# Kernel optimization log

Hardware: AMD Instinct MI355X
Metric: run time of the kernel (lower is better)

Reference implementation:

```python
import jax, jax.numpy as jnp
import numpy as np

B, T, D, K = 8, 2048, 384, 64

def setup_inputs() -> dict:
    key = jax.random.key(0)
    k1, k2, k3, k4 = jax.random.split(key, 4)
    x = jax.random.normal(k1, (B, T, D), dtype=jnp.float32)
    # torch nn.Linear default init scale ~ 1/sqrt(fan_in); use scaled normals
    Wq = jax.random.normal(k2, (D, K), dtype=jnp.float32) / np.sqrt(D)
    Wk = jax.random.normal(k3, (D, K), dtype=jnp.float32) / np.sqrt(D)
    Wv = jax.random.normal(k4, (D, D), dtype=jnp.float32) / np.sqrt(D)
    return {"x": x, "Wq": Wq, "Wk": Wk, "Wv": Wv}

def reference(x, Wq, Wk, Wv):
    # x: (B,T,D)
    q = jnp.einsum('btd,dk->btk', x, Wq)      # (B,T,K)
    k = jnp.einsum('btd,dk->btk', x, Wk)      # (B,T,K)
    v = jnp.einsum('btd,de->bte', x, Wv)      # (B,T,D)
    scores = jnp.einsum('bqk,bsk->bqs', q, k) / jnp.sqrt(jnp.float32(K))  # (B,T,T)
    causal = jnp.tril(jnp.ones((T, T), dtype=bool))
    scores = jnp.where(causal, scores, -jnp.inf)
    weights = jax.nn.softmax(scores, axis=-1)
    out = jnp.einsum('bqs,bse->bqe', weights, v)  # (B,T,D)
    return out
```

## Files before the change

kernel.cpp:

```cpp
#include <hip/hip_runtime.h>

#define TT 2048
#define DD 384

typedef float f32x4 __attribute__((ext_vector_type(4)));
typedef float f32x16 __attribute__((ext_vector_type(16)));
typedef short s16x8 __attribute__((ext_vector_type(8)));
typedef short s16x2 __attribute__((ext_vector_type(2)));
typedef unsigned int u32x4 __attribute__((ext_vector_type(4)));

typedef __attribute__((address_space(3))) unsigned char* as3p;
typedef const __attribute__((address_space(1))) unsigned char* as1p;
#define GLLDS(gsrc, ldst) __builtin_amdgcn_global_load_lds((as1p)(gsrc), (as3p)(ldst), 16, 0, 0)

static __device__ __forceinline__ unsigned short f2bf(float f) {
    unsigned int u = __builtin_bit_cast(unsigned int, f);
    u = (u + 0x7fffu + ((u >> 16) & 1u)) >> 16;
    return (unsigned short)u;
}
static __device__ __forceinline__ unsigned int pk2(float a, float b) {
#if __has_builtin(__builtin_amdgcn_cvt_pk_bf16_f32)
    s16x2 t = __builtin_amdgcn_cvt_pk_bf16_f32(a, b);
    return __builtin_bit_cast(unsigned int, t);
#else
    unsigned int ua = __builtin_bit_cast(unsigned int, a);
    unsigned int ub = __builtin_bit_cast(unsigned int, b);
    ua = (ua + 0x7fffu + ((ua >> 16) & 1u)) >> 16;
    ub = (ub + 0x7fffu + ((ub >> 16) & 1u)) & 0xffff0000u;
    return ua | ub;
#endif
}

__global__ __launch_bounds__(256, 2) void qkv_gemm(
    const float* __restrict__ x, const float* __restrict__ Wq,
    const float* __restrict__ Wk, const float* __restrict__ Wv,
    unsigned short* __restrict__ qo, unsigned short* __restrict__ ko,
    unsigned short* __restrict__ vto)
{
    __shared__ __align__(16) unsigned short lds[16384];
    const int tid = threadIdx.x;
    const int l   = tid & 63;
    const int w   = tid >> 6;
    const int si  = l & 15;
    const int qq  = l >> 4;
    const int m0  = blockIdx.x * 128;
    const int nb  = blockIdx.y;
    const int wr  = w >> 1, wc = w & 1;

    const int bn = tid & 127;
    const int bk = (tid >> 7) * 16;
    const float* wsrc; int ldw;
    if (nb == 0) { wsrc = (bn < 64) ? (Wq + bn) : (Wk + (bn - 64)); ldw = 64; }
    else         { wsrc = Wv + (nb - 1) * 128 + bn;                 ldw = 384; }

    f32x4 acc[4][4];
    #pragma unroll
    for (int rt = 0; rt < 4; ++rt)
        #pragma unroll
        for (int ct = 0; ct < 4; ++ct) acc[rt][ct] = (f32x4){0.f, 0.f, 0.f, 0.f};

    for (int kt = 0; kt < 12; ++kt) {
        const int k0 = kt * 32;
        #pragma unroll
        for (int i = 0; i < 2; ++i) {
            const int u = tid + 256 * i, r = u >> 2, c = u & 3;
            const float* xp = x + (size_t)(m0 + r) * DD + k0 + c * 8;
            f32x4 x0 = *(const f32x4*)xp;
            f32x4 x1 = *(const f32x4*)(xp + 4);
            s16x8 av;
            av[0] = (short)f2bf(x0[0]); av[1] = (short)f2bf(x0[1]);
            av[2] = (short)f2bf(x0[2]); av[3] = (short)f2bf(x0[3]);
            av[4] = (short)f2bf(x1[0]); av[5] = (short)f2bf(x1[1]);
            av[6] = (short)f2bf(x1[2]); av[7] = (short)f2bf(x1[3]);
            *(s16x8*)&lds[r * 32 + ((c ^ (r & 3)) * 8)] = av;
        }
        {
            float t[16];
            #pragma unroll
            for (int j = 0; j < 16; ++j) t[j] = wsrc[(size_t)(k0 + bk + j) * ldw];
            #pragma unroll
            for (int jj = 0; jj < 2; ++jj) {
                s16x8 bv;
                #pragma unroll
                for (int j = 0; j < 8; ++j) bv[j] = (short)f2bf(t[jj * 8 + j]);
                const int ch = (tid >> 7) * 2 + jj;
                *(s16x8*)&lds[4096 + bn * 32 + ((ch ^ (bn & 3)) * 8)] = bv;
            }
        }
        __syncthreads();

        s16x8 af[4], bf[4];
        #pragma unroll
        for (int rt = 0; rt < 4; ++rt) {
            const int row = wr * 64 + rt * 16 + si;
            af[rt] = *(const s16x8*)&lds[row * 32 + ((qq ^ (row & 3)) * 8)];
        }
        #pragma unroll
        for (int ct = 0; ct < 4; ++ct) {
            const int col = wc * 64 + ct * 16 + si;
            bf[ct] = *(const s16x8*)&lds[4096 + col * 32 + ((qq ^ (col & 3)) * 8)];
        }
        #pragma unroll
        for (int rt = 0; rt < 4; ++rt)
            #pragma unroll
            for (int ct = 0; ct < 4; ++ct)
                acc[rt][ct] = __builtin_amdgcn_mfma_f32_16x16x32_bf16(af[rt], bf[ct], acc[rt][ct], 0, 0, 0);
        __syncthreads();
    }

    if (nb == 0) {
        if (wc == 0) {
            #pragma unroll
            for (int rt = 0; rt < 4; ++rt)
                #pragma unroll
                for (int ct = 0; ct < 4; ++ct)
                    #pragma unroll
                    for (int r = 0; r < 4; ++r) {
                        const int m = m0 + wr * 64 + rt * 16 + qq * 4 + r;
                        qo[(size_t)m * 64 + ct * 16 + si] = f2bf(acc[rt][ct][r] * 0.125f);
                    }
        } else {
            #pragma unroll
            for (int rt = 0; rt < 4; ++rt)
                #pragma unroll
                for (int ct = 0; ct < 4; ++ct)
                    #pragma unroll
                    for (int r = 0; r < 4; ++r) {
                        const int m = m0 + wr * 64 + rt * 16 + qq * 4 + r;
                        const int col = ct * 16 + si;
                        ko[(size_t)m * 64 + (((col >> 3) ^ (m & 7)) * 8) + (col & 7)] = f2bf(acc[rt][ct][r]);
                    }
        }
    } else {
        #pragma unroll
        for (int rt = 0; rt < 4; ++rt)
            #pragma unroll
            for (int ct = 0; ct < 4; ++ct)
                #pragma unroll
                for (int r = 0; r < 4; ++r) {
                    const int m = wr * 64 + rt * 16 + qq * 4 + r;
                    const int n = wc * 64 + ct * 16 + si;
                    lds[n * 128 + (((m >> 3) ^ (n & 7)) * 8) + (m & 7)] = f2bf(acc[rt][ct][r]);
                }
        __syncthreads();
        const int bbat = m0 >> 11, t0 = m0 & 2047;
        #pragma unroll
        for (int i = 0; i < 8; ++i) {
            const int u = tid + 256 * i, n = u >> 4, mc = u & 15;
            s16x8 v = *(const s16x8*)&lds[n * 128 + ((mc ^ (n & 7)) * 8)];
            *(s16x8*)&vto[((size_t)bbat * DD + ((nb - 1) * 128 + n)) * TT
                          + t0 + (mc >> 3) * 64 + (((mc & 7) ^ (n & 7)) * 8)] = v;
        }
    }
}

__global__ __launch_bounds__(512, 4) void attn(
    const unsigned short* __restrict__ qg, const unsigned short* __restrict__ kg,
    const unsigned short* __restrict__ vg, float* __restrict__ out)
{
    __shared__ __align__(16) unsigned short lds[40960];

    const int tid = threadIdx.x;
    const int l   = tid & 63;
    const int w   = tid >> 6;
    const int par = w >> 2;
    const int qb  = w & 3;
    const int lo  = l & 31;
    const int hi  = l >> 5;

    const int g  = blockIdx.x;
    const int bb = g & 7;
    const int eq = (g >> 3) & 3;
    const int jidx = g >> 5;
    const int j  = (g < 256) ? jidx : (23 - jidx);
    const int q0 = j * 128;
    const int e0 = eq * 96;
    const int qrow = q0 + qb * 32 + lo;

    s16x8 qf[4];
    {
        const unsigned short* qp = qg + ((size_t)bb * TT + qrow) * 64;
        #pragma unroll
        for (int st = 0; st < 4; ++st) qf[st] = *(const s16x8*)(qp + st * 16 + hi * 8);
    }

    f32x16 o[3];
    #pragma unroll
    for (int et = 0; et < 3; ++et)
        #pragma unroll
        for (int r = 0; r < 16; ++r) o[et][r] = 0.f;
    float lp = 0.f;

    const unsigned short* kbase = kg + (size_t)bb * TT * 64;
    const unsigned short* vbase = vg + ((size_t)bb * DD + e0) * TT;

    #define STAGE(IT, BUF)                                                                  \
    {                                                                                       \
        const unsigned short* kb = kbase + (size_t)(IT) * 128 * 64;                         \
        unsigned short* kl = &lds[(BUF) * 8192];                                            \
        GLLDS(kb + (2 * w) * 512 + l * 8,     &kl[(2 * w) * 512]);                          \
        GLLDS(kb + (2 * w + 1) * 512 + l * 8, &kl[(2 * w + 1) * 512]);                      \
        unsigned short* vl = &lds[16384 + (BUF) * 12288];                                   \
        _Pragma("unroll")                                                                   \
        for (int c3 = 0; c3 < 3; ++c3) {                                                    \
            const int ch = 3 * w + c3;                                                      \
            const int p = ch / 12, rr = (ch % 12) * 8;                                      \
            const unsigned short* vb = vbase + ((size_t)(rr + (l >> 3))) * TT               \
                                       + (IT) * 128 + p * 64 + (l & 7) * 8;                 \
            GLLDS(vb, &vl[ch * 512]);                                                       \
        }                                                                                   \
    }

    STAGE(0, 0);

    for (int it = 0; it <= j; ++it) {
        const int buf = it & 1;
        __syncthreads();

        if (it < j) STAGE(it + 1, 1 - buf);

        const unsigned short* Ks = &lds[buf * 8192 + par * 4096];
        const unsigned short* Vs = &lds[16384 + buf * 12288 + par * 6144];

        const int s0 = (2 * it + par) * 64;
        if (s0 <= q0 + qb * 32 + 31) {
            const bool mb = (s0 + 63 > q0 + qb * 32);
            #pragma unroll
            for (int ct = 0; ct < 2; ++ct) {
                f32x16 sa;
                #pragma unroll
                for (int r = 0; r < 16; ++r) sa[r] = 0.f;
                #pragma unroll
                for (int st = 0; st < 4; ++st) {
                    s16x8 kf = *(const s16x8*)&Ks[(ct * 32 + lo) * 64 + (((st * 2 + hi) ^ (lo & 7)) * 8)];
                    sa = __builtin_amdgcn_mfma_f32_32x32x16_bf16(kf, qf[st], sa, 0, 0, 0);
                }
                float pv[16];
                #pragma unroll
                for (int r = 0; r < 16; ++r) {
                    float e = __expf(sa[r]);
                    if (mb) {
                        const int srow = s0 + ct * 32 + (r & 3) + 8 * (r >> 2) + 4 * hi;
                        if (srow > qrow) e = 0.f;
                    }
                    pv[r] = e;
                    lp += e;
                }
                unsigned int d0 = pk2(pv[0], pv[1]),   d1 = pk2(pv[2], pv[3]);
                unsigned int d2 = pk2(pv[4], pv[5]),   d3 = pk2(pv[6], pv[7]);
                unsigned int d4 = pk2(pv[8], pv[9]),   d5 = pk2(pv[10], pv[11]);
                unsigned int d6 = pk2(pv[12], pv[13]), d7 = pk2(pv[14], pv[15]);
                unsigned int sA0 = hi ? d0 : d2, sA1 = hi ? d1 : d3;
                unsigned int rA0 = (unsigned int)__shfl_xor((int)sA0, 32);
                unsigned int rA1 = (unsigned int)__shfl_xor((int)sA1, 32);
                u32x4 fa0 = hi ? (u32x4){rA0, rA1, d2, d3} : (u32x4){d0, d1, rA0, rA1};
                unsigned int sB0 = hi ? d4 : d6, sB1 = hi ? d5 : d7;
                unsigned int rB0 = (unsigned int)__shfl_xor((int)sB0, 32);
                unsigned int rB1 = (unsigned int)__shfl_xor((int)sB1, 32);
                u32x4 fa1 = hi ? (u32x4){rB0, rB1, d6, d7} : (u32x4){d4, d5, rB0, rB1};
                s16x8 a0 = __builtin_bit_cast(s16x8, fa0);
                s16x8 a1 = __builtin_bit_cast(s16x8, fa1);
                #pragma unroll
                for (int et = 0; et < 3; ++et) {
                    const int el = et * 32 + lo;
                    s16x8 v0 = *(const s16x8*)&Vs[el * 64 + (((ct * 4 + hi) ^ (el & 7)) * 8)];
                    o[et] = __builtin_amdgcn_mfma_f32_32x32x16_bf16(a0, v0, o[et], 0, 0, 0);
                    s16x8 v1 = *(const s16x8*)&Vs[el * 64 + (((ct * 4 + 2 + hi) ^ (el & 7)) * 8)];
                    o[et] = __builtin_amdgcn_mfma_f32_32x32x16_bf16(a1, v1, o[et], 0, 0, 0);
                }
            }
        }
    }
    __syncthreads();

    float* fb  = (float*)lds;
    float* stL = (float*)lds + 6144;
    lp += __shfl_xor(lp, 32);
    if (hi == 0) stL[par * 128 + qb * 32 + lo] = lp;
    __syncthreads();

    #pragma unroll
    for (int ph = 0; ph < 2; ++ph) {
        if (par == 1 && (qb >> 1) == ph) {
            const int slot = qb & 1;
            #pragma unroll
            for (int r = 0; r < 16; ++r) {
                const int rloc = (r & 3) + 8 * (r >> 2) + 4 * hi;
                #pragma unroll
                for (int et = 0; et < 3; ++et)
                    fb[slot * 3072 + rloc * 96 + et * 32 + lo] = o[et][r];
            }
        }
        __syncthreads();
        if (par == 0 && (qb >> 1) == ph) {
            const int slot = qb & 1;
            #pragma unroll
            for (int r = 0; r < 16; ++r) {
                const int rloc = (r & 3) + 8 * (r >> 2) + 4 * hi;
                const float linv = 1.f / (stL[qb * 32 + rloc] + stL[128 + qb * 32 + rloc]);
                float* op = out + ((size_t)bb * TT + q0 + qb * 32 + rloc) * DD + e0;
                #pragma unroll
                for (int et = 0; et < 3; ++et)
                    op[et * 32 + lo] = (o[et][r] + fb[slot * 3072 + rloc * 96 + et * 32 + lo]) * linv;
            }
        }
        __syncthreads();
    }
}

extern "C" void kernel_launch(void* const* d_in, const int* in_sizes, int n_in,
                              void* d_out, int out_size, void* d_ws, size_t ws_size,
                              hipStream_t stream)
{
    const float* x  = (const float*)d_in[0];
    const float* Wq = (const float*)d_in[1];
    const float* Wk = (const float*)d_in[2];
    const float* Wv = (const float*)d_in[3];

    unsigned short* qws  = (unsigned short*)d_ws;
    unsigned short* kws  = (unsigned short*)((char*)d_ws + ((size_t)2 << 20));
    unsigned short* vtws = (unsigned short*)((char*)d_ws + ((size_t)4 << 20));

    qkv_gemm<<<dim3(128, 4), dim3(256), 0, stream>>>(x, Wq, Wk, Wv, qws, kws, vtws);
    attn<<<dim3(512), dim3(512), 0, stream>>>(qws, kws, vtws, (float*)d_out);
}
```

Measured before the change: 143.2 us.

## Split attention key tiles across four wave groups with 1024-thread blocks

Doubles the attention block to 1024 threads so four wave groups each handle one 32-key slice of every 128-key tile, instead of two groups looping over two slices. Staging is spread across 16 waves and the final reduction now combines three partial outputs and four row sums through LDS. The block order changes to a plain longest-first schedule in place of the paired causal balancing. This adds more parallel waves to hide latency, at the cost of more register pressure, larger cross-wave reductions, and possibly worse load balance.

```diff
diff --git a/kernel.cpp b/kernel.cpp
--- a/kernel.cpp
+++ b/kernel.cpp
@@ -154,7 +154,7 @@
     }
 }
 
-__global__ __launch_bounds__(512, 4) void attn(
+__global__ __launch_bounds__(1024, 4) void attn(
     const unsigned short* __restrict__ qg, const unsigned short* __restrict__ kg,
     const unsigned short* __restrict__ vg, float* __restrict__ out)
 {
@@ -163,16 +163,17 @@
     const int tid = threadIdx.x;
     const int l   = tid & 63;
     const int w   = tid >> 6;
-    const int par = w >> 2;
+    const int q4  = w >> 2;
     const int qb  = w & 3;
     const int lo  = l & 31;
     const int hi  = l >> 5;
+    const int h   = q4 >> 1;
+    const int ct  = q4 & 1;
 
     const int g  = blockIdx.x;
     const int bb = g & 7;
     const int eq = (g >> 3) & 3;
-    const int jidx = g >> 5;
-    const int j  = (g < 256) ? jidx : (23 - jidx);
+    const int j  = 15 - (g >> 5);
     const int q0 = j * 128;
     const int e0 = eq * 96;
     const int qrow = q0 + qb * 32 + lo;
@@ -194,21 +195,19 @@
     const unsigned short* kbase = kg + (size_t)bb * TT * 64;
     const unsigned short* vbase = vg + ((size_t)bb * DD + e0) * TT;
 
-    #define STAGE(IT, BUF)                                                                  \
-    {                                                                                       \
-        const unsigned short* kb = kbase + (size_t)(IT) * 128 * 64;                         \
-        unsigned short* kl = &lds[(BUF) * 8192];                                            \
-        GLLDS(kb + (2 * w) * 512 + l * 8,     &kl[(2 * w) * 512]);                          \
-        GLLDS(kb + (2 * w + 1) * 512 + l * 8, &kl[(2 * w + 1) * 512]);                      \
-        unsigned short* vl = &lds[16384 + (BUF) * 12288];                                   \
-        _Pragma("unroll")                                                                   \
-        for (int c3 = 0; c3 < 3; ++c3) {                                                    \
-            const int ch = 3 * w + c3;                                                      \
-            const int p = ch / 12, rr = (ch % 12) * 8;                                      \
-            const unsigned short* vb = vbase + ((size_t)(rr + (l >> 3))) * TT               \
-                                       + (IT) * 128 + p * 64 + (l & 7) * 8;                 \
-            GLLDS(vb, &vl[ch * 512]);                                                       \
-        }                                                                                   \
+    const unsigned short* kS = kbase + w * 512 + l * 8;
+    const int chA = w,      pA = chA / 12, rrA = (chA % 12) * 8;
+    const int chB = 16 + w, pB = chB / 12, rrB = (chB % 12) * 8;
+    const unsigned short* vSA = vbase + ((size_t)(rrA + (l >> 3))) * TT + pA * 64 + (l & 7) * 8;
+    const unsigned short* vSB = vbase + ((size_t)(rrB + (l >> 3))) * TT + pB * 64 + (l & 7) * 8;
+
+    #define STAGE(IT, BUF)                                                   \
+    {                                                                        \
+        unsigned short* kl = &lds[(BUF) * 8192];                             \
+        GLLDS(kS + (size_t)(IT) * 8192, &kl[w * 512]);                       \
+        unsigned short* vl = &lds[16384 + (BUF) * 12288];                    \
+        GLLDS(vSA + (IT) * 128, &vl[chA * 512]);                             \
+        if (w < 8) GLLDS(vSB + (IT) * 128, &vl[chB * 512]);                  \
     }
 
     STAGE(0, 0);
@@ -219,93 +218,95 @@
 
         if (it < j) STAGE(it + 1, 1 - buf);
 
-        const unsigned short* Ks = &lds[buf * 8192 + par * 4096];
-        const unsigned short* Vs = &lds[16384 + buf * 12288 + par * 6144];
-
-        const int s0 = (2 * it + par) * 64;
-        if (s0 <= q0 + qb * 32 + 31) {
-            const bool mb = (s0 + 63 > q0 + qb * 32);
-            #pragma unroll
-            for (int ct = 0; ct < 2; ++ct) {
-                f32x16 sa;
-                #pragma unroll
-                for (int r = 0; r < 16; ++r) sa[r] = 0.f;
-                #pragma unroll
-                for (int st = 0; st < 4; ++st) {
-                    s16x8 kf = *(const s16x8*)&Ks[(ct * 32 + lo) * 64 + (((st * 2 + hi) ^ (lo & 7)) * 8)];
-                    sa = __builtin_amdgcn_mfma_f32_32x32x16_bf16(kf, qf[st], sa, 0, 0, 0);
+        const unsigned short* Ks = &lds[buf * 8192 + h * 4096];
+        const unsigned short* Vs = &lds[16384 + buf * 12288 + h * 6144];
+
+        const int sq = it * 128 + q4 * 32;
+        if (sq <= q0 + qb * 32 + 31) {
+            const bool mb = (sq + 31 > q0 + qb * 32);
+            f32x16 sa;
+            #pragma unroll
+            for (int r = 0; r < 16; ++r) sa[r] = 0.f;
+            #pragma unroll
+            for (int st = 0; st < 4; ++st) {
+                s16x8 kf = *(const s16x8*)&Ks[(ct * 32 + lo) * 64 + (((st * 2 + hi) ^ (lo & 7)) * 8)];
+                sa = __builtin_amdgcn_mfma_f32_32x32x16_bf16(kf, qf[st], sa, 0, 0, 0);
+            }
+            float pv[16];
+            #pragma unroll
+            for (int r = 0; r < 16; ++r) {
+                float e = __expf(sa[r]);
+                if (mb) {
+                    const int srow = sq + (r & 3) + 8 * (r >> 2) + 4 * hi;
+                    if (srow > qrow) e = 0.f;
                 }
-                float pv[16];
-                #pragma unroll
-                for (int r = 0; r < 16; ++r) {
-                    float e = __expf(sa[r]);
-                    if (mb) {
-                        const int srow = s0 + ct * 32 + (r & 3) + 8 * (r >> 2) + 4 * hi;
-                        if (srow > qrow) e = 0.f;
-                    }
-                    pv[r] = e;
-                    lp += e;
-                }
-                unsigned int d0 = pk2(pv[0], pv[1]),   d1 = pk2(pv[2], pv[3]);
-                unsigned int d2 = pk2(pv[4], pv[5]),   d3 = pk2(pv[6], pv[7]);
-                unsigned int d4 = pk2(pv[8], pv[9]),   d5 = pk2(pv[10], pv[11]);
-                unsigned int d6 = pk2(pv[12], pv[13]), d7 = pk2(pv[14], pv[15]);
-                unsigned int sA0 = hi ? d0 : d2, sA1 = hi ? d1 : d3;
-                unsigned int rA0 = (unsigned int)__shfl_xor((int)sA0, 32);
-                unsigned int rA1 = (unsigned int)__shfl_xor((int)sA1, 32);
-                u32x4 fa0 = hi ? (u32x4){rA0, rA1, d2, d3} : (u32x4){d0, d1, rA0, rA1};
-                unsigned int sB0 = hi ? d4 : d6, sB1 = hi ? d5 : d7;
-                unsigned int rB0 = (unsigned int)__shfl_xor((int)sB0, 32);
-                unsigned int rB1 = (unsigned int)__shfl_xor((int)sB1, 32);
-                u32x4 fa1 = hi ? (u32x4){rB0, rB1, d6, d7} : (u32x4){d4, d5, rB0, rB1};
-                s16x8 a0 = __builtin_bit_cast(s16x8, fa0);
-                s16x8 a1 = __builtin_bit_cast(s16x8, fa1);
-                #pragma unroll
-                for (int et = 0; et < 3; ++et) {
-                    const int el = et * 32 + lo;
-                    s16x8 v0 = *(const s16x8*)&Vs[el * 64 + (((ct * 4 + hi) ^ (el & 7)) * 8)];
-                    o[et] = __builtin_amdgcn_mfma_f32_32x32x16_bf16(a0, v0, o[et], 0, 0, 0);
-                    s16x8 v1 = *(const s16x8*)&Vs[el * 64 + (((ct * 4 + 2 + hi) ^ (el & 7)) * 8)];
-                    o[et] = __builtin_amdgcn_mfma_f32_32x32x16_bf16(a1, v1, o[et], 0, 0, 0);
-                }
+                pv[r] = e;
+                lp += e;
+            }
+            unsigned int d0 = pk2(pv[0], pv[1]),   d1 = pk2(pv[2], pv[3]);
+            unsigned int d2 = pk2(pv[4], pv[5]),   d3 = pk2(pv[6], pv[7]);
+            unsigned int d4 = pk2(pv[8], pv[9]),   d5 = pk2(pv[10], pv[11]);
+            unsigned int d6 = pk2(pv[12], pv[13]), d7 = pk2(pv[14], pv[15]);
+            unsigned int sA0 = hi ? d0 : d2, sA1 = hi ? d1 : d3;
+            unsigned int rA0 = (unsigned int)__shfl_xor((int)sA0, 32);
+            unsigned int rA1 = (unsigned int)__shfl_xor((int)sA1, 32);
+            u32x4 fa0 = hi ? (u32x4){rA0, rA1, d2, d3} : (u32x4){d0, d1, rA0, rA1};
+            unsigned int sB0 = hi ? d4 : d6, sB1 = hi ? d5 : d7;
+            unsigned int rB0 = (unsigned int)__shfl_xor((int)sB0, 32);
+            unsigned int rB1 = (unsigned int)__shfl_xor((int)sB1, 32);
+            u32x4 fa1 = hi ? (u32x4){rB0, rB1, d6, d7} : (u32x4){d4, d5, rB0, rB1};
+            s16x8 a0 = __builtin_bit_cast(s16x8, fa0);
+            s16x8 a1 = __builtin_bit_cast(s16x8, fa1);
+            #pragma unroll
+            for (int et = 0; et < 3; ++et) {
+                const int el = et * 32 + lo;
+                s16x8 v0 = *(const s16x8*)&Vs[el * 64 + (((ct * 4 + hi) ^ (el & 7)) * 8)];
+                o[et] = __builtin_amdgcn_mfma_f32_32x32x16_bf16(a0, v0, o[et], 0, 0, 0);
+                s16x8 v1 = *(const s16x8*)&Vs[el * 64 + (((ct * 4 + 2 + hi) ^ (el & 7)) * 8)];
+                o[et] = __builtin_amdgcn_mfma_f32_32x32x16_bf16(a1, v1, o[et], 0, 0, 0);
             }
         }
     }
     __syncthreads();
 
-    float* fb  = (float*)lds;
-    float* stL = (float*)lds + 6144;
+    float* stL = (float*)lds;
+    float* fb  = (float*)lds + 512;
     lp += __shfl_xor(lp, 32);
-    if (hi == 0) stL[par * 128 + qb * 32 + lo] = lp;
+    if (hi == 0) stL[q4 * 128 + qb * 32 + lo] = lp;
     __syncthreads();
 
     #pragma unroll
     for (int ph = 0; ph < 2; ++ph) {
-        if (par == 1 && (qb >> 1) == ph) {
-            const int slot = qb & 1;
+        if (q4 != 0 && (qb >> 1) == ph) {
+            const int slot = (q4 - 1) * 64 + (qb & 1) * 32;
             #pragma unroll
             for (int r = 0; r < 16; ++r) {
                 const int rloc = (r & 3) + 8 * (r >> 2) + 4 * hi;
                 #pragma unroll
                 for (int et = 0; et < 3; ++et)
-                    fb[slot * 3072 + rloc * 96 + et * 32 + lo] = o[et][r];
-            }
-        }
-        __syncthreads();
-        if (par == 0 && (qb >> 1) == ph) {
-            const int slot = qb & 1;
+                    fb[(slot + rloc) * 96 + et * 32 + lo] = o[et][r];
+            }
+        }
+        __syncthreads();
+        if (q4 == 0 && (qb >> 1) == ph) {
+            const int slot = (qb & 1) * 32;
             #pragma unroll
             for (int r = 0; r < 16; ++r) {
                 const int rloc = (r & 3) + 8 * (r >> 2) + 4 * hi;
-                const float linv = 1.f / (stL[qb * 32 + rloc] + stL[128 + qb * 32 + rloc]);
-                float* op = out + ((size_t)bb * TT + q0 + qb * 32 + rloc) * DD + e0;
+                const int rr = qb * 32 + rloc;
+                const float linv = 1.f / (stL[rr] + stL[128 + rr] + stL[256 + rr] + stL[384 + rr]);
+                float* op = out + ((size_t)bb * TT + q0 + rr) * DD + e0;
                 #pragma unroll
                 for (int et = 0; et < 3; ++et)
-                    op[et * 32 + lo] = (o[et][r] + fb[slot * 3072 + rloc * 96 + et * 32 + lo]) * linv;
-            }
-        }
-        __syncthreads();
-    }
+                    op[et * 32 + lo] = (o[et][r]
+                        + fb[(0 * 64 + slot + rloc) * 96 + et * 32 + lo]
+                        + fb[(1 * 64 + slot + rloc) * 96 + et * 32 + lo]
+                        + fb[(2 * 64 + slot + rloc) * 96 + et * 32 + lo]) * linv;
+            }
+        }
+        __syncthreads();
+    }
+    #undef STAGE
 }
 
 extern "C" void kernel_launch(void* const* d_in, const int* in_sizes, int n_in,
@@ -322,5 +323,5 @@
     unsigned short* vtws = (unsigned short*)((char*)d_ws + ((size_t)4 << 20));
 
     qkv_gemm<<<dim3(128, 4), dim3(256), 0, stream>>>(x, Wq, Wk, Wv, qws, kws, vtws);
-    attn<<<dim3(512), dim3(512), 0, stream>>>(qws, kws, vtws, (float*)d_out);
-}
+    attn<<<dim3(512), dim3(1024), 0, stream>>>(qws, kws, vtws, (float*)d_out);
+}
```

Result: slower. 150.4 us (+5.0%).
